# Kernel optimization log

Hardware: AMD Instinct MI355X
Metric: run time of the kernel (lower is better)

## Reference

```python
import jax, jax.numpy as jnp
import numpy as np

KERNEL = (8, 8)
STRIDE = (4, 4)


def setup_inputs() -> dict:
    key = jax.random.key(0)
    x = jax.random.normal(key, (8, 32, 8, 8, 4096), dtype=jnp.float32)
    return {"x": x}


def reference(x):
    b, c, k1, k2, l = x.shape
    s1, s2 = STRIDE
    n = round(l ** 0.5)  # patch grid is n x n (row-major: i outer, j inner)
    h = s1 * (n - 1) + k1
    w = s2 * (n - 1) + k2
    # b c k1 k2 (n n) -> indexable per kernel offset
    xp = x.reshape(b, c, k1, k2, n, n)
    out = jnp.zeros((b, c, h, w), dtype=x.dtype)
    # For a fixed kernel offset (di, dj), the target positions p*s+di are a
    # non-overlapping strided slice, so each add is a disjoint scatter.
    for di in range(k1):
        for dj in range(k2):
            out = out.at[:, :, di:di + s1 * n:s1, dj:dj + s2 * n:s2].add(
                xp[:, :, di, dj])
    return out
```

## Files before the change

kernel.cpp:

```cpp
#include <hip/hip_runtime.h>


#define L      4096
#define NP     64
#define H_OUT  260

typedef float vfloat4 __attribute__((ext_vector_type(4)));

__device__ __forceinline__ float elem(const vfloat4& v, int e) {
    return v[e];
}

__global__ __launch_bounds__(256) void fold_kernel(const float* __restrict__ x,
                                                   float* __restrict__ out) {
    int tid  = blockIdx.x * 256 + threadIdx.x;
    int lane = tid & 63;
    int wave = tid >> 6;

    int g    = wave % 17;
    int rest = wave / 17;
    int r    = rest & 3;
    int bc   = rest >> 2;

    int q  = lane & 15;
    int io = lane >> 4;
    int ip = 4 * g + io;

    bool va = (ip < NP);
    bool vb = (ip >= 1) && (ip <= NP);

    int xb   = bc * (64 * L);
    int aoff = xb + r       * (8 * L) + ip       * NP + 4 * q;
    int boff = xb + (r + 4) * (8 * L) + (ip - 1) * NP + 4 * q;

    const vfloat4 z4 = (vfloat4){0.f, 0.f, 0.f, 0.f};
    vfloat4 A[8], B[8];
    #pragma unroll
    for (int dj = 0; dj < 8; ++dj) {
        A[dj] = va ? *reinterpret_cast<const vfloat4*>(x + aoff + dj * L) : z4;
        B[dj] = vb ? *reinterpret_cast<const vfloat4*>(x + boff + dj * L) : z4;
    }

    float sa[4], sb[4];
    #pragma unroll
    for (int s = 0; s < 4; ++s) {
        float ta = __shfl_up(A[4 + s][3], 1);
        float tb = __shfl_up(B[4 + s][3], 1);
        sa[s] = (q == 0) ? 0.f : ta;
        sb[s] = (q == 0) ? 0.f : tb;
    }

    if (ip <= NP) {
        int h  = 4 * ip + r;
        int ob = (bc * H_OUT + h) * H_OUT + 16 * q;

        #pragma unroll
        for (int e = 0; e < 4; ++e) {
            vfloat4 v;
            #pragma unroll
            for (int s = 0; s < 4; ++s) {
                float lo = elem(A[s], e) + elem(B[s], e);
                float hi_a = (e == 0) ? sa[s] : elem(A[4 + s], e - 1);
                float hi_b = (e == 0) ? sb[s] : elem(B[4 + s], e - 1);
                v[s] = lo + (hi_a + hi_b);
            }
            *reinterpret_cast<vfloat4*>(out + ob + 4 * e) = v;
        }

        if (q == 15) {
            vfloat4 v = (vfloat4){A[4][3] + B[4][3],
                                  A[5][3] + B[5][3],
                                  A[6][3] + B[6][3],
                                  A[7][3] + B[7][3]};
            *reinterpret_cast<vfloat4*>(out + ob + 16) = v;
        }
    }
}

extern "C" void kernel_launch(void* const* d_in, const int* in_sizes, int n_in,
                              void* d_out, int out_size, void* d_ws, size_t ws_size,
                              hipStream_t stream) {
    const float* x = (const float*)d_in[0];
    float* out     = (float*)d_out;

    const int grid  = 17408 / 4;
    const int block = 256;

    fold_kernel<<<grid, block, 0, stream>>>(x, out);
}
```

Before: 385.0 us.

## Stage fold inputs through LDS via async global_load_lds and remap blocks

Replaces per-thread strided vector loads and cross-lane shuffles with block-level async global-to-LDS copies (global_load_lds) of 16 input planes per block. Each thread then reads its A/B neighbours from LDS and writes a full 64-float output row segment. The grid is remapped to 4096 blocks of 16 patch rows each, and a special tail path handles the last output row (ip=64). This trades register pressure and 64 KB of LDS per block (lower occupancy) for contiguous coalesced global loads.

```diff
diff --git a/kernel.cpp b/kernel.cpp
--- a/kernel.cpp
+++ b/kernel.cpp
@@ -7,73 +7,92 @@
 
 typedef float vfloat4 __attribute__((ext_vector_type(4)));
 
-__device__ __forceinline__ float elem(const vfloat4& v, int e) {
-    return v[e];
-}
-
 __global__ __launch_bounds__(256) void fold_kernel(const float* __restrict__ x,
                                                    float* __restrict__ out) {
-    int tid  = blockIdx.x * 256 + threadIdx.x;
-    int lane = tid & 63;
-    int wave = tid >> 6;
+    __shared__ float lds[16384];
 
-    int g    = wave % 17;
-    int rest = wave / 17;
-    int r    = rest & 3;
-    int bc   = rest >> 2;
+    int bid = blockIdx.x;
+    int G   = bid & 3;
+    int r   = (bid >> 2) & 3;
+    int bc  = bid >> 4;
 
-    int q  = lane & 15;
-    int io = lane >> 4;
-    int ip = 4 * g + io;
+    int lane = threadIdx.x & 63;
+    int wv   = threadIdx.x >> 6;
 
-    bool va = (ip < NP);
-    bool vb = (ip >= 1) && (ip <= NP);
+    #pragma unroll
+    for (int ci = 0; ci < 4; ++ci) {
+        int c   = 4 * wv + ci;
+        int isB = c >> 3;
+        int p   = c & 7;
+        int di  = r + 4 * isB;
+        long gb = ((long)(bc * 64 + di * 8 + p)) * L + (long)(16 * G - isB) * 64;
+        const float* gp = x + gb + lane * 4;
+        float* lp = lds + c * 1024;
+        #pragma unroll
+        for (int k = 0; k < 4; ++k) {
+            __builtin_amdgcn_global_load_lds(
+                (const __attribute__((address_space(1))) void*)(gp + k * 256),
+                (__attribute__((address_space(3))) void*)(lp + k * 256),
+                16, 0, 0);
+        }
+    }
+    __syncthreads();
 
-    int xb   = bc * (64 * L);
-    int aoff = xb + r       * (8 * L) + ip       * NP + 4 * q;
-    int boff = xb + (r + 4) * (8 * L) + (ip - 1) * NP + 4 * q;
+    int t  = threadIdx.x;
+    int ii = t >> 4;
+    int ug = t & 15;
+    int ip = 16 * G + ii;
+    bool bvalid = (ip >= 1);
 
-    const vfloat4 z4 = (vfloat4){0.f, 0.f, 0.f, 0.f};
-    vfloat4 A[8], B[8];
+    const vfloat4* l4 = (const vfloat4*)lds;
+    const vfloat4 vz = {0.f, 0.f, 0.f, 0.f};
+
+    vfloat4 o[4];
+    float tl[4];
+
     #pragma unroll
-    for (int dj = 0; dj < 8; ++dj) {
-        A[dj] = va ? *reinterpret_cast<const vfloat4*>(x + aoff + dj * L) : z4;
-        B[dj] = vb ? *reinterpret_cast<const vfloat4*>(x + boff + dj * L) : z4;
+    for (int s = 0; s < 4; ++s) {
+        int ai = s * 256 + ii * 16 + ug;
+        int bi = 2048 + ai;
+        int ahi = (s + 4) * 256 + ii * 16 + ug;
+        int bhi = 2048 + ahi;
+
+        vfloat4 alo = l4[ai];
+        vfloat4 blo = bvalid ? l4[bi] : vz;
+        vfloat4 ahc = l4[ahi];
+        vfloat4 bhc = bvalid ? l4[bhi] : vz;
+        float ahp = (ug > 0) ? l4[ahi - 1][3] : 0.f;
+        float bhp = (ug > 0 && bvalid) ? l4[bhi - 1][3] : 0.f;
+
+        o[0][s] = alo[0] + blo[0] + ahp    + bhp;
+        o[1][s] = alo[1] + blo[1] + ahc[0] + bhc[0];
+        o[2][s] = alo[2] + blo[2] + ahc[1] + bhc[1];
+        o[3][s] = alo[3] + blo[3] + ahc[2] + bhc[2];
+        tl[s]   = ahc[3] + bhc[3];
     }
 
-    float sa[4], sb[4];
-    #pragma unroll
-    for (int s = 0; s < 4; ++s) {
-        float ta = __shfl_up(A[4 + s][3], 1);
-        float tb = __shfl_up(B[4 + s][3], 1);
-        sa[s] = (q == 0) ? 0.f : ta;
-        sb[s] = (q == 0) ? 0.f : tb;
+    long orow = ((long)(bc * H_OUT) + (4 * ip + r)) * H_OUT;
+    vfloat4* op = (vfloat4*)(out + orow);
+    op[4 * ug + 0] = o[0];
+    op[4 * ug + 1] = o[1];
+    op[4 * ug + 2] = o[2];
+    op[4 * ug + 3] = o[3];
+    if (ug == 15) {
+        vfloat4 tv = {tl[0], tl[1], tl[2], tl[3]};
+        op[64] = tv;
     }
 
-    if (ip <= NP) {
-        int h  = 4 * ip + r;
-        int ob = (bc * H_OUT + h) * H_OUT + 16 * q;
-
+    if (G == 3 && t < 65) {
+        int u = t;
+        const float* pb = x + ((long)(bc * 64 + (r + 4) * 8)) * L + 63 * 64;
+        vfloat4 v;
         #pragma unroll
-        for (int e = 0; e < 4; ++e) {
-            vfloat4 v;
-            #pragma unroll
-            for (int s = 0; s < 4; ++s) {
-                float lo = elem(A[s], e) + elem(B[s], e);
-                float hi_a = (e == 0) ? sa[s] : elem(A[4 + s], e - 1);
-                float hi_b = (e == 0) ? sb[s] : elem(B[4 + s], e - 1);
-                v[s] = lo + (hi_a + hi_b);
-            }
-            *reinterpret_cast<vfloat4*>(out + ob + 4 * e) = v;
+        for (int s = 0; s < 4; ++s) {
+            float lo = (u <= 63) ? pb[(long)s * L + u] : 0.f;
+            float hi = (u >= 1) ? pb[(long)(s + 4) * L + u - 1] : 0.f;
+            v[s] = lo + hi;
         }
-
-        if (q == 15) {
-            vfloat4 v = (vfloat4){A[4][3] + B[4][3],
-                                  A[5][3] + B[5][3],
-                                  A[6][3] + B[6][3],
-                                  A[7][3] + B[7][3]};
-            *reinterpret_cast<vfloat4*>(out + ob + 16) = v;
-        }
+        ((vfloat4*)(out + ((long)(bc * H_OUT) + 256 + r) * H_OUT))[u] = v;
     }
 }
 
@@ -83,8 +102,5 @@
     const float* x = (const float*)d_in[0];
     float* out     = (float*)d_out;
 
-    const int grid  = 17408 / 4;
-    const int block = 256;
-
-    fold_kernel<<<grid, block, 0, stream>>>(x, out);
+    fold_kernel<<<4096, 256, 0, stream>>>(x, out);
 }
```

Result: faster. 369.7 us (-4.0%).
